# Performance work log

Measured on AMD Instinct MI355X. Metric: run time of the kernel, lower is better.

## Reference

```python
import jax, jax.numpy as jnp
import numpy as np

B, S, T, F, H, DEPTH = 8, 96, 96, 64, 64, 2


def setup_inputs() -> dict:
    key = jax.random.key(0)
    ks = jax.random.split(key, 10)
    scale = np.float32(1.0 / np.sqrt(H))
    rn = lambda k, sh: jax.random.normal(k, sh, dtype=jnp.float32)
    return {
        "src": rn(ks[0], (B, S, F)),
        "trg": rn(ks[1], (B, T, F)),
        "Wi_x": rn(ks[2], (DEPTH, F, H)) * scale,
        "Wh_x": rn(ks[3], (DEPTH, 2 * H, H)) * scale,
        "b_x": jnp.zeros((DEPTH, H), jnp.float32),
        "Wi_y": rn(ks[4], (DEPTH, F, H)) * scale,
        "Wh_y": rn(ks[5], (DEPTH, 2 * H, H)) * scale,
        "b_y": jnp.zeros((DEPTH, H), jnp.float32),
        "src_lens": jax.random.randint(ks[6], (B,), 1, S + 1),
        "trg_lens": jax.random.randint(ks[7], (B,), 1, T + 1),
    }


def _grid_layer(px, py, Whx, bx, Why, by):
    # px, py: (B, S, T, H) precomputed input projections (x @ Wi).
    # Wavefront recurrence: h_prev = [h_x(i-1,j), h_y(i,j-1)] (zeros at borders),
    # h_x(i,j) = tanh(px + h_prev @ Whx + bx), h_y(i,j) = tanh(py + h_prev @ Why + by).
    Bn, Sn, Tn, Hn = px.shape

    def row_step(hx_above_row, row_in):
        pxr, pyr = row_in  # (T, B, H) each

        def col_step(hy_left, col_in):
            pxc, pyc, hx_above = col_in  # (B, H) each
            h_prev = jnp.concatenate([hx_above, hy_left], axis=-1)  # (B, 2H)
            hx = jnp.tanh(pxc + h_prev @ Whx + bx)
            hy = jnp.tanh(pyc + h_prev @ Why + by)
            return hy, (hx, hy)

        _, (hx_row, hy_row) = jax.lax.scan(
            col_step, jnp.zeros((Bn, Hn), px.dtype), (pxr, pyr, hx_above_row))
        return hx_row, (hx_row, hy_row)

    px_t = jnp.transpose(px, (1, 2, 0, 3))  # (S, T, B, H)
    py_t = jnp.transpose(py, (1, 2, 0, 3))
    _, (hx, hy) = jax.lax.scan(
        row_step, jnp.zeros((Tn, Bn, Hn), px.dtype), (px_t, py_t))
    return jnp.transpose(hx, (2, 0, 1, 3)), jnp.transpose(hy, (2, 0, 1, 3))


def _forward(src, trg, Wi_x, Wh_x, b_x, Wi_y, Wh_y, b_y, src_lens, trg_lens):
    hx = hy = None
    hxs, hys = [], []
    for d in range(DEPTH):
        if d == 0:
            # depth 0: x input depends only on i, y input only on j
            px = jnp.broadcast_to((src @ Wi_x[0])[:, :, None, :], (B, S, T, H))
            py = jnp.broadcast_to((trg @ Wi_y[0])[:, None, :, :], (B, S, T, H))
        else:
            # depth d>0: inputs are previous depth's x/y outputs at the same (i,j)
            px = jnp.einsum('bsth,hk->bstk', hx, Wi_x[d])
            py = jnp.einsum('bsth,hk->bstk', hy, Wi_y[d])
        hx, hy = _grid_layer(px, py, Wh_x[d], b_x[d], Wh_y[d], b_y[d])
        hxs.append(hx)
        hys.append(hy)
    # zero out points outside each sample's (src_len x trg_len) valid grid
    mask = ((jnp.arange(S)[None, :, None] < src_lens[:, None, None])
            & (jnp.arange(T)[None, None, :] < trg_lens[:, None, None]))
    mask = mask[:, :, :, None].astype(src.dtype)  # (B, S, T, 1)
    out = jnp.stack([jnp.stack(hxs), jnp.stack(hys)])  # (2, DEPTH, B, S, T, H)
    return out * mask


_forward_jit = jax.jit(_forward)


def reference(src, trg, Wi_x, Wh_x, b_x, Wi_y, Wh_y, b_y, src_lens, trg_lens):
    return _forward_jit(src, trg, Wi_x, Wh_x, b_x, Wi_y, Wh_y, b_y,
                        src_lens, trg_lens)
```

## Files before the change

### kernel.cpp

```cpp
#include <hip/hip_runtime.h>

typedef unsigned short u16;
typedef unsigned int   u32;
typedef _Float16 f16x8 __attribute__((ext_vector_type(8)));
typedef float  f32x4  __attribute__((ext_vector_type(4)));
typedef int    i32x4  __attribute__((ext_vector_type(4)));
typedef u32    u32x2  __attribute__((ext_vector_type(2)));

#define Bn 8
#define Sn 96
#define Tn 96
#define Hn 64
#define H2n 128
#define STRB 144
#define ARRB 16384
#define LDSB (8*ARRB)

__device__ __forceinline__ int imax(int a, int b){ return a > b ? a : b; }
__device__ __forceinline__ int imin(int a, int b){ return a < b ? a : b; }

__device__ __forceinline__ u32 pack2f16(float a, float b){
  _Float16 ha = (_Float16)a, hb = (_Float16)b;
  return (u32)__builtin_bit_cast(u16, ha) | ((u32)__builtin_bit_cast(u16, hb) << 16);
}
__device__ __forceinline__ float fast_tanh(float x){
  float y = fminf(fmaxf(x * 2.88539008f, -30.f), 30.f);
  float e = __builtin_amdgcn_exp2f(y);
  return __builtin_fmaf(-2.f, __builtin_amdgcn_rcpf(e + 1.f), 1.f);
}
__device__ __forceinline__ void barrier_lds_only(){
  asm volatile("s_waitcnt vmcnt(63) expcnt(7) lgkmcnt(0)\n\ts_barrier" ::: "memory");
}

__global__ __launch_bounds__(64) void proj0_kernel(
  const float* __restrict__ src, const float* __restrict__ trg,
  const float* __restrict__ Wix, const float* __restrict__ Wiy,
  const float* __restrict__ bx, const float* __restrict__ by,
  float* __restrict__ ws)
{
  const int row = blockIdx.x, g = blockIdx.y, b = blockIdx.z;
  const int n = threadIdx.x;
  const float* x = (g == 0) ? (src + (b*Sn + row)*Hn) : (trg + (b*Tn + row)*Hn);
  const float* W = (g == 0) ? Wix : Wiy;
  float a = (g == 0) ? bx[n] : by[n];
  #pragma unroll 8
  for (int f = 0; f < Hn; ++f) a = fmaf(x[f], W[f*Hn + n], a);
  ws[((size_t)(b*2 + g)*Sn + row)*Hn + n] = a;
}

__global__ __launch_bounds__(1024, 1) void grid_rnn_fused(
  const float* __restrict__ Whx, const float* __restrict__ Why,
  const float* __restrict__ Wix, const float* __restrict__ Wiy,
  const float* __restrict__ bx,  const float* __restrict__ by,
  const int* __restrict__ src_lens, const int* __restrict__ trg_lens,
  float* __restrict__ out, const float* __restrict__ ws)
{
  extern __shared__ u16 smem[];
  char* const smemc = (char*)smem;
  const int b    = blockIdx.x;
  const int tid  = threadIdx.x;
  const int lane = tid & 63;
  const int wid  = __builtin_amdgcn_readfirstlane(tid >> 6);
  const int q    = lane >> 4;
  const int c    = lane & 15;
  const int dep  = wid & 1;
  const int nt   = (wid >> 1) & 3;
  const int g    = wid >> 3;
  const int sl = __builtin_amdgcn_readfirstlane(src_lens[b]);
  const int tl = __builtin_amdgcn_readfirstlane(trg_lens[b]);
  const int NB = sl + tl;

  for (int idx = tid; idx < LDSB/4; idx += 1024) ((u32*)smem)[idx] = 0u;

  const float* Wh = (g == 0 ? Whx : Why) + dep*H2n*Hn;
  const int nb = nt*16 + c;
  i32x4 whf[4];
  #pragma unroll
  for (int kk = 0; kk < 4; ++kk){
    #pragma unroll
    for (int p = 0; p < 4; ++p){
      float w0 = Wh[(kk*32 + q*8 + 2*p    )*Hn + nb];
      float w1 = Wh[(kk*32 + q*8 + 2*p + 1)*Hn + nb];
      whf[kk][p] = (int)pack2f16(w0, w1);
    }
  }
  const float* Wi = (g == 0 ? Wix : Wiy) + Hn*Hn;
  i32x4 wif[2];
  #pragma unroll
  for (int kk = 0; kk < 2; ++kk){
    #pragma unroll
    for (int p = 0; p < 4; ++p){
      float w0 = Wi[(kk*32 + q*8 + 2*p    )*Hn + nb];
      float w1 = Wi[(kk*32 + q*8 + 2*p + 1)*Hn + nb];
      wif[kk][p] = (int)pack2f16(w0, w1);
    }
  }
  f32x4 bias4;
  {
    const float* bb = (g == 0 ? bx : by) + dep*Hn;
    #pragma unroll
    for (int r4 = 0; r4 < 4; ++r4) bias4[r4] = bb[nt*16 + q*4 + r4];
  }
  const char* const pxb = (const char*)(ws + (size_t)(b*2 + g)*Sn*Hn);
  char* const outb = (char*)(out + (size_t)((g*2 + dep)*Bn + b)*(size_t)(Sn*Tn)*Hn);

  const int plJ = q*16 - c*STRB;
  const int plI = q*16 + c*STRB;
  const int plP = g ? plI : plJ;
  const int plW = (g ? c*STRB : -c*STRB) + nt*32 + q*8;
  const int plO = c*24320 + nt*64 + q*16;
  const int plPx= (g ? -c*256 : c*256) + nt*64 + q*16;

  const int baseX = dep*4*ARRB;
  const int baseY = dep*4*ARRB + 2*ARRB;
  const int baseP = g ? 2*ARRB : 0;
  const int baseW = dep*4*ARRB + (g ? 2*ARRB : 0);

  __syncthreads();

  for (int r = 0; r < NB; ++r){
    const int myd  = r - dep;
    const bool wact = (myd >= 0) && (myd <= NB - 2);
    const int cpB = (r & 1) ? ARRB : 0;
    const int ppB = ARRB - cpB;
    const int i0 = imax(0, myd - (tl - 1));
    const int i1 = imin(sl - 1, myd);
    const int nc = i1 - i0 + 1;
    const int mtiles = (nc + 15) >> 4;
    const int sJ = (myd - i0)*STRB;
    const int sI = i0*STRB;
    const int aX  = baseX + ppB + sJ;
    const int loX = baseX + ppB + (myd - i1)*STRB;
    const int aY  = baseY + ppB + sI;
    const int hiY = baseY + ppB + i1*STRB + 48;
    const int aP  = baseP + ppB + (g ? sI : sJ);
    const int loP = baseP + ppB + (g ? sI : (myd - i1)*STRB);
    const int hiP = baseP + ppB + (g ? i1*STRB : sJ) + 48;
    const int aW  = baseW + cpB + (g ? sI : sJ);
    const int sO  = myd*256 + i0*24320;
    const int sPx = (g ? (myd - i0) : i0)*256;
    const int pxLo= (g ? (myd - i1) : i0)*256;
    const int pxHi= (g ? (myd - i0) : i1)*256 + 240;

    #pragma unroll
    for (int u = 0; u < 6; ++u){
      if (!(wact && u < mtiles)) continue;
      const int du = u*2304;
      int vX = aX - du + plJ; vX = imax(vX, loX);
      int vY = aY + du + plI; vY = imin(vY, hiY);

      f32x4 acc;
      if (dep == 0){
        int vp = (g ? sPx - u*4096 : sPx + u*4096) + plPx;
        vp = imin(imax(vp, pxLo), pxHi);
        acc = *(const f32x4*)(pxb + (u32)vp);
      } else {
        acc = bias4;
      }
      #pragma unroll
      for (int kk = 0; kk < 2; ++kk){
        i32x4 sv = *(const i32x4*)(smemc + (vX + kk*64));
        acc = __builtin_amdgcn_mfma_f32_16x16x32_f16(
                __builtin_bit_cast(f16x8, whf[kk]),
                __builtin_bit_cast(f16x8, sv), acc, 0, 0, 0);
      }
      #pragma unroll
      for (int kk = 0; kk < 2; ++kk){
        i32x4 sv = *(const i32x4*)(smemc + (vY + kk*64));
        acc = __builtin_amdgcn_mfma_f32_16x16x32_f16(
                __builtin_bit_cast(f16x8, whf[kk+2]),
                __builtin_bit_cast(f16x8, sv), acc, 0, 0, 0);
      }
      if (dep == 1){
        int vP = aP + (g ? du : -du) + plP;
        vP = imin(imax(vP, loP), hiP);
        #pragma unroll
        for (int kk = 0; kk < 2; ++kk){
          i32x4 pv = *(const i32x4*)(smemc + (vP + kk*64));
          acc = __builtin_amdgcn_mfma_f32_16x16x32_f16(
                  __builtin_bit_cast(f16x8, wif[kk]),
                  __builtin_bit_cast(f16x8, pv), acc, 0, 0, 0);
        }
      }
      float h0 = fast_tanh(acc[0]), h1 = fast_tanh(acc[1]);
      float h2 = fast_tanh(acc[2]), h3 = fast_tanh(acc[3]);
      if (c < nc - u*16){
        int vW = aW + (g ? du : -du) + plW;
        u32x2 hp; hp[0] = pack2f16(h0, h1); hp[1] = pack2f16(h2, h3);
        *(u32x2*)(smemc + vW) = hp;
        int vO = sO + u*389120 + plO;
        f32x4 ov = {h0, h1, h2, h3};
        *(f32x4*)(outb + (u32)vO) = ov;
      }
    }
    barrier_lds_only();
  }
}

extern "C" void kernel_launch(void* const* d_in, const int* in_sizes, int n_in,
                              void* d_out, int out_size, void* d_ws, size_t ws_size,
                              hipStream_t stream) {
  (void)in_sizes; (void)n_in; (void)ws_size;
  (void)hipFuncSetAttribute((const void*)grid_rnn_fused,
                            hipFuncAttributeMaxDynamicSharedMemorySize, LDSB);
  (void)hipMemsetAsync(d_out, 0, (size_t)out_size, stream);
  proj0_kernel<<<dim3(Sn, 2, Bn), 64, 0, stream>>>(
      (const float*)d_in[0], (const float*)d_in[1],
      (const float*)d_in[2], (const float*)d_in[5],
      (const float*)d_in[4], (const float*)d_in[7],
      (float*)d_ws);
  grid_rnn_fused<<<dim3(Bn), dim3(1024), LDSB, stream>>>(
      (const float*)d_in[3], (const float*)d_in[6],
      (const float*)d_in[2], (const float*)d_in[5],
      (const float*)d_in[4], (const float*)d_in[7],
      (const int*)d_in[8], (const int*)d_in[9],
      (float*)d_out, (const float*)d_ws);
}
```

Before: 526.8 us.

## Switch wavefront recurrence to 32x32x16 MFMA tiles with 512-thread blocks

Replaces the 16x16x32 MFMA tiling, where each wave computed a 16-column slice of one cell batch, with 32x32x16 MFMA tiles in which each wave computes all 64 outputs for 32 diagonal cells. The block shrinks from 16 to 8 waves, each wave alternating between tiles. The LDS row stride moves to 152 bytes and state is read with paired 8-byte loads, aiming to cut bank conflicts. The clamp in tanh is dropped. The goal is fewer MFMA instructions and fewer redundant state loads per step, at the cost of more registers per wave, less wave-level parallelism and lower MFMA utilisation on short diagonals.

```diff
diff --git a/kernel.cpp b/kernel.cpp
--- a/kernel.cpp
+++ b/kernel.cpp
@@ -4,6 +4,7 @@
 typedef unsigned int   u32;
 typedef _Float16 f16x8 __attribute__((ext_vector_type(8)));
 typedef float  f32x4  __attribute__((ext_vector_type(4)));
+typedef float  f32x16 __attribute__((ext_vector_type(16)));
 typedef int    i32x4  __attribute__((ext_vector_type(4)));
 typedef u32    u32x2  __attribute__((ext_vector_type(2)));
 
@@ -12,9 +13,10 @@
 #define Tn 96
 #define Hn 64
 #define H2n 128
-#define STRB 144
+#define STRB 152
 #define ARRB 16384
 #define LDSB (8*ARRB)
+#define ODS 24320
 
 __device__ __forceinline__ int imax(int a, int b){ return a > b ? a : b; }
 __device__ __forceinline__ int imin(int a, int b){ return a < b ? a : b; }
@@ -24,12 +26,17 @@
   return (u32)__builtin_bit_cast(u16, ha) | ((u32)__builtin_bit_cast(u16, hb) << 16);
 }
 __device__ __forceinline__ float fast_tanh(float x){
-  float y = fminf(fmaxf(x * 2.88539008f, -30.f), 30.f);
-  float e = __builtin_amdgcn_exp2f(y);
+  float e = exp2f(x * 2.88539008f);
   return __builtin_fmaf(-2.f, __builtin_amdgcn_rcpf(e + 1.f), 1.f);
 }
 __device__ __forceinline__ void barrier_lds_only(){
   asm volatile("s_waitcnt vmcnt(63) expcnt(7) lgkmcnt(0)\n\ts_barrier" ::: "memory");
+}
+__device__ __forceinline__ f16x8 ld_state(const char* p){
+  u32x2 a = *(const u32x2*)(p);
+  u32x2 b = *(const u32x2*)(p + 8);
+  i32x4 v; v[0] = (int)a[0]; v[1] = (int)a[1]; v[2] = (int)b[0]; v[3] = (int)b[1];
+  return __builtin_bit_cast(f16x8, v);
 }
 
 __global__ __launch_bounds__(64) void proj0_kernel(
@@ -48,7 +55,7 @@
   ws[((size_t)(b*2 + g)*Sn + row)*Hn + n] = a;
 }
 
-__global__ __launch_bounds__(1024, 1) void grid_rnn_fused(
+__global__ __launch_bounds__(512, 2) void grid_rnn_fused(
   const float* __restrict__ Whx, const float* __restrict__ Why,
   const float* __restrict__ Wix, const float* __restrict__ Wiy,
   const float* __restrict__ bx,  const float* __restrict__ by,
@@ -61,60 +68,63 @@
   const int tid  = threadIdx.x;
   const int lane = tid & 63;
   const int wid  = __builtin_amdgcn_readfirstlane(tid >> 6);
-  const int q    = lane >> 4;
-  const int c    = lane & 15;
+  const int c32  = lane & 31;
+  const int hi   = lane >> 5;
   const int dep  = wid & 1;
-  const int nt   = (wid >> 1) & 3;
-  const int g    = wid >> 3;
+  const int g    = (wid >> 1) & 1;
+  const int ct   = (wid >> 2) & 1;
   const int sl = __builtin_amdgcn_readfirstlane(src_lens[b]);
   const int tl = __builtin_amdgcn_readfirstlane(trg_lens[b]);
   const int NB = sl + tl;
 
-  for (int idx = tid; idx < LDSB/4; idx += 1024) ((u32*)smem)[idx] = 0u;
+  for (int idx = tid; idx < LDSB/4; idx += 512) ((u32*)smem)[idx] = 0u;
 
   const float* Wh = (g == 0 ? Whx : Why) + dep*H2n*Hn;
-  const int nb = nt*16 + c;
-  i32x4 whf[4];
+  i32x4 whf[8][2];
   #pragma unroll
-  for (int kk = 0; kk < 4; ++kk){
-    #pragma unroll
-    for (int p = 0; p < 4; ++p){
-      float w0 = Wh[(kk*32 + q*8 + 2*p    )*Hn + nb];
-      float w1 = Wh[(kk*32 + q*8 + 2*p + 1)*Hn + nb];
-      whf[kk][p] = (int)pack2f16(w0, w1);
-    }
-  }
-  const float* Wi = (g == 0 ? Wix : Wiy) + Hn*Hn;
-  i32x4 wif[2];
-  #pragma unroll
-  for (int kk = 0; kk < 2; ++kk){
-    #pragma unroll
-    for (int p = 0; p < 4; ++p){
-      float w0 = Wi[(kk*32 + q*8 + 2*p    )*Hn + nb];
-      float w1 = Wi[(kk*32 + q*8 + 2*p + 1)*Hn + nb];
-      wif[kk][p] = (int)pack2f16(w0, w1);
-    }
-  }
-  f32x4 bias4;
-  {
-    const float* bb = (g == 0 ? bx : by) + dep*Hn;
-    #pragma unroll
-    for (int r4 = 0; r4 < 4; ++r4) bias4[r4] = bb[nt*16 + q*4 + r4];
+  for (int kk = 0; kk < 8; ++kk)
+    #pragma unroll
+    for (int mt = 0; mt < 2; ++mt)
+      #pragma unroll
+      for (int p = 0; p < 4; ++p){
+        float w0 = Wh[(kk*16 + hi*8 + 2*p    )*Hn + mt*32 + c32];
+        float w1 = Wh[(kk*16 + hi*8 + 2*p + 1)*Hn + mt*32 + c32];
+        whf[kk][mt][p] = (int)pack2f16(w0, w1);
+      }
+  i32x4 wif[4][2];
+  f32x16 biasr[2];
+  if (dep == 1){
+    const float* Wi = (g == 0 ? Wix : Wiy) + Hn*Hn;
+    #pragma unroll
+    for (int kk = 0; kk < 4; ++kk)
+      #pragma unroll
+      for (int mt = 0; mt < 2; ++mt)
+        #pragma unroll
+        for (int p = 0; p < 4; ++p){
+          float w0 = Wi[(kk*16 + hi*8 + 2*p    )*Hn + mt*32 + c32];
+          float w1 = Wi[(kk*16 + hi*8 + 2*p + 1)*Hn + mt*32 + c32];
+          wif[kk][mt][p] = (int)pack2f16(w0, w1);
+        }
+    const float* bb = (g == 0 ? bx : by) + Hn;
+    #pragma unroll
+    for (int mt = 0; mt < 2; ++mt)
+      #pragma unroll
+      for (int reg = 0; reg < 16; ++reg)
+        biasr[mt][reg] = bb[mt*32 + (reg & 3) + 8*(reg >> 2) + 4*hi];
   }
   const char* const pxb = (const char*)(ws + (size_t)(b*2 + g)*Sn*Hn);
   char* const outb = (char*)(out + (size_t)((g*2 + dep)*Bn + b)*(size_t)(Sn*Tn)*Hn);
 
-  const int plJ = q*16 - c*STRB;
-  const int plI = q*16 + c*STRB;
-  const int plP = g ? plI : plJ;
-  const int plW = (g ? c*STRB : -c*STRB) + nt*32 + q*8;
-  const int plO = c*24320 + nt*64 + q*16;
-  const int plPx= (g ? -c*256 : c*256) + nt*64 + q*16;
-
-  const int baseX = dep*4*ARRB;
-  const int baseY = dep*4*ARRB + 2*ARRB;
-  const int baseP = g ? 2*ARRB : 0;
-  const int baseW = dep*4*ARRB + (g ? 2*ARRB : 0);
+  const int plX  = -c32*STRB + hi*16;
+  const int plY  =  c32*STRB + hi*16;
+  const int plP  = g ? plY : plX;
+  const int plW  = (g ? c32*STRB : -c32*STRB) + hi*8;
+  const int plO  = c32*ODS + hi*16;
+  const int plPx = (g ? -c32*256 : c32*256) + hi*16;
+
+  const int depB  = dep*4*ARRB;
+  const int basePg = g ? 2*ARRB : 0;
+  const int baseWg = depB + (g ? 2*ARRB : 0);
 
   __syncthreads();
 
@@ -126,71 +136,88 @@
     const int i0 = imax(0, myd - (tl - 1));
     const int i1 = imin(sl - 1, myd);
     const int nc = i1 - i0 + 1;
-    const int mtiles = (nc + 15) >> 4;
-    const int sJ = (myd - i0)*STRB;
-    const int sI = i0*STRB;
-    const int aX  = baseX + ppB + sJ;
-    const int loX = baseX + ppB + (myd - i1)*STRB;
-    const int aY  = baseY + ppB + sI;
-    const int hiY = baseY + ppB + i1*STRB + 48;
-    const int aP  = baseP + ppB + (g ? sI : sJ);
-    const int loP = baseP + ppB + (g ? sI : (myd - i1)*STRB);
-    const int hiP = baseP + ppB + (g ? i1*STRB : sJ) + 48;
-    const int aW  = baseW + cpB + (g ? sI : sJ);
-    const int sO  = myd*256 + i0*24320;
-    const int sPx = (g ? (myd - i0) : i0)*256;
-    const int pxLo= (g ? (myd - i1) : i0)*256;
-    const int pxHi= (g ? (myd - i0) : i1)*256 + 240;
-
-    #pragma unroll
-    for (int u = 0; u < 6; ++u){
-      if (!(wact && u < mtiles)) continue;
-      const int du = u*2304;
-      int vX = aX - du + plJ; vX = imax(vX, loX);
-      int vY = aY + du + plI; vY = imin(vY, hiY);
-
-      f32x4 acc;
+    const int mt32 = (nc + 31) >> 5;
+    const int rJ0 = myd - i0, rJm = myd - i1;
+    const int aX  = depB + ppB + rJ0*STRB;
+    const int loX = depB + ppB + rJm*STRB;
+    const int aY  = depB + 2*ARRB + ppB + i0*STRB;
+    const int hiY = depB + 2*ARRB + ppB + i1*STRB + 16;
+    const int aP  = basePg + ppB + (g ? i0 : rJ0)*STRB;
+    const int loP = basePg + ppB + (g ? i0 : rJm)*STRB;
+    const int hiP = basePg + ppB + (g ? i1 : rJ0)*STRB + 16;
+    const int aW  = baseWg + cpB + (g ? i0 : rJ0)*STRB;
+    const int sO  = myd*256 + i0*ODS;
+    const int sPx = (g ? rJ0 : i0)*256;
+    const int loPx= (g ? rJm : i0)*256;
+    const int hiPx= (g ? rJ0 : i1)*256 + 16;
+
+    #pragma unroll
+    for (int t = 0; t < 2; ++t){
+      const int u = ct + 2*t;
+      if (!(wact && u < mt32)) continue;
+      const int cb = u*32;
+
+      int vX = aX - cb*STRB + plX; vX = imax(vX, loX);
+      int vY = aY + cb*STRB + plY; vY = imin(vY, hiY);
+
+      f32x16 acc[2];
       if (dep == 0){
-        int vp = (g ? sPx - u*4096 : sPx + u*4096) + plPx;
-        vp = imin(imax(vp, pxLo), pxHi);
-        acc = *(const f32x4*)(pxb + (u32)vp);
+        int vp = sPx + (g ? -(cb*256) : cb*256) + plPx;
+        vp = imin(imax(vp, loPx), hiPx);
+        #pragma unroll
+        for (int m = 0; m < 4; ++m){
+          f32x4 t0 = *(const f32x4*)(pxb + (u32)vp + m*32);
+          f32x4 t1 = *(const f32x4*)(pxb + (u32)vp + 128 + m*32);
+          #pragma unroll
+          for (int e = 0; e < 4; ++e){ acc[0][4*m+e] = t0[e]; acc[1][4*m+e] = t1[e]; }
+        }
       } else {
-        acc = bias4;
-      }
-      #pragma unroll
-      for (int kk = 0; kk < 2; ++kk){
-        i32x4 sv = *(const i32x4*)(smemc + (vX + kk*64));
-        acc = __builtin_amdgcn_mfma_f32_16x16x32_f16(
-                __builtin_bit_cast(f16x8, whf[kk]),
-                __builtin_bit_cast(f16x8, sv), acc, 0, 0, 0);
-      }
-      #pragma unroll
-      for (int kk = 0; kk < 2; ++kk){
-        i32x4 sv = *(const i32x4*)(smemc + (vY + kk*64));
-        acc = __builtin_amdgcn_mfma_f32_16x16x32_f16(
-                __builtin_bit_cast(f16x8, whf[kk+2]),
-                __builtin_bit_cast(f16x8, sv), acc, 0, 0, 0);
+        acc[0] = biasr[0]; acc[1] = biasr[1];
+      }
+      #pragma unroll
+      for (int kk = 0; kk < 4; ++kk){
+        f16x8 bv = ld_state(smemc + vX + kk*32);
+        acc[0] = __builtin_amdgcn_mfma_f32_32x32x16_f16(
+                   __builtin_bit_cast(f16x8, whf[kk][0]), bv, acc[0], 0, 0, 0);
+        acc[1] = __builtin_amdgcn_mfma_f32_32x32x16_f16(
+                   __builtin_bit_cast(f16x8, whf[kk][1]), bv, acc[1], 0, 0, 0);
+      }
+      #pragma unroll
+      for (int kk = 0; kk < 4; ++kk){
+        f16x8 bv = ld_state(smemc + vY + kk*32);
+        acc[0] = __builtin_amdgcn_mfma_f32_32x32x16_f16(
+                   __builtin_bit_cast(f16x8, whf[kk+4][0]), bv, acc[0], 0, 0, 0);
+        acc[1] = __builtin_amdgcn_mfma_f32_32x32x16_f16(
+                   __builtin_bit_cast(f16x8, whf[kk+4][1]), bv, acc[1], 0, 0, 0);
       }
       if (dep == 1){
-        int vP = aP + (g ? du : -du) + plP;
+        int vP = aP + (g ? cb*STRB : -(cb*STRB)) + plP;
         vP = imin(imax(vP, loP), hiP);
         #pragma unroll
-        for (int kk = 0; kk < 2; ++kk){
-          i32x4 pv = *(const i32x4*)(smemc + (vP + kk*64));
-          acc = __builtin_amdgcn_mfma_f32_16x16x32_f16(
-                  __builtin_bit_cast(f16x8, wif[kk]),
-                  __builtin_bit_cast(f16x8, pv), acc, 0, 0, 0);
+        for (int kk = 0; kk < 4; ++kk){
+          f16x8 pv = ld_state(smemc + vP + kk*32);
+          acc[0] = __builtin_amdgcn_mfma_f32_32x32x16_f16(
+                     __builtin_bit_cast(f16x8, wif[kk][0]), pv, acc[0], 0, 0, 0);
+          acc[1] = __builtin_amdgcn_mfma_f32_32x32x16_f16(
+                     __builtin_bit_cast(f16x8, wif[kk][1]), pv, acc[1], 0, 0, 0);
         }
       }
-      float h0 = fast_tanh(acc[0]), h1 = fast_tanh(acc[1]);
-      float h2 = fast_tanh(acc[2]), h3 = fast_tanh(acc[3]);
-      if (c < nc - u*16){
-        int vW = aW + (g ? du : -du) + plW;
-        u32x2 hp; hp[0] = pack2f16(h0, h1); hp[1] = pack2f16(h2, h3);
-        *(u32x2*)(smemc + vW) = hp;
-        int vO = sO + u*389120 + plO;
-        f32x4 ov = {h0, h1, h2, h3};
-        *(f32x4*)(outb + (u32)vO) = ov;
+      if (c32 < nc - cb){
+        const int vW = aW + (g ? cb*STRB : -(cb*STRB)) + plW;
+        const int vO = sO + cb*ODS + plO;
+        #pragma unroll
+        for (int mt = 0; mt < 2; ++mt)
+          #pragma unroll
+          for (int m = 0; m < 4; ++m){
+            float h0 = fast_tanh(acc[mt][4*m+0]);
+            float h1 = fast_tanh(acc[mt][4*m+1]);
+            float h2 = fast_tanh(acc[mt][4*m+2]);
+            float h3 = fast_tanh(acc[mt][4*m+3]);
+            u32x2 hp; hp[0] = pack2f16(h0, h1); hp[1] = pack2f16(h2, h3);
+            *(u32x2*)(smemc + vW + mt*64 + m*16) = hp;
+            f32x4 ov = {h0, h1, h2, h3};
+            *(f32x4*)(outb + (u32)vO + mt*128 + m*32) = ov;
+          }
       }
     }
     barrier_lds_only();
@@ -209,7 +236,7 @@
       (const float*)d_in[2], (const float*)d_in[5],
       (const float*)d_in[4], (const float*)d_in[7],
       (float*)d_ws);
-  grid_rnn_fused<<<dim3(Bn), dim3(1024), LDSB, stream>>>(
+  grid_rnn_fused<<<dim3(Bn), dim3(512), LDSB, stream>>>(
       (const float*)d_in[3], (const float*)d_in[6],
       (const float*)d_in[2], (const float*)d_in[5],
       (const float*)d_in[4], (const float*)d_in[7],
```

After: 608.8 us. +15.6%, slower.

## Stage depth-0 input projections in LDS as fp16 and pad state stride

Applied to the files above, without the earlier changes.

The depth-0 input projections are copied once from the workspace into LDS as packed fp16 rows, and the wavefront loop reads them from LDS instead of global memory. The LDS state row stride changes from 144 to 152 bytes, which alters bank mapping. tanh drops its input clamp and uses exp2f. Rounding px to fp16 adds precision loss, and removing the clamp depends on exp2f overflowing to infinity and rcp of infinity giving zero.

```diff
diff --git a/kernel.cpp b/kernel.cpp
--- a/kernel.cpp
+++ b/kernel.cpp
@@ -3,6 +3,7 @@
 typedef unsigned short u16;
 typedef unsigned int   u32;
 typedef _Float16 f16x8 __attribute__((ext_vector_type(8)));
+typedef float  f32x2  __attribute__((ext_vector_type(2)));
 typedef float  f32x4  __attribute__((ext_vector_type(4)));
 typedef int    i32x4  __attribute__((ext_vector_type(4)));
 typedef u32    u32x2  __attribute__((ext_vector_type(2)));
@@ -12,9 +13,15 @@
 #define Tn 96
 #define Hn 64
 #define H2n 128
-#define STRB 144
+#define STRB 152
 #define ARRB 16384
-#define LDSB (8*ARRB)
+#define STATEB 131072
+#define PXROW 152
+#define PXG   (Sn*PXROW)
+#define PXBASE STATEB
+#define LDSB  (STATEB + 2*PXG)
+#define ODS 24320
+#define TSTP 2432
 
 __device__ __forceinline__ int imax(int a, int b){ return a > b ? a : b; }
 __device__ __forceinline__ int imin(int a, int b){ return a < b ? a : b; }
@@ -23,9 +30,11 @@
   _Float16 ha = (_Float16)a, hb = (_Float16)b;
   return (u32)__builtin_bit_cast(u16, ha) | ((u32)__builtin_bit_cast(u16, hb) << 16);
 }
+__device__ __forceinline__ float f16tof(u32 v){
+  return (float)__builtin_bit_cast(_Float16, (u16)v);
+}
 __device__ __forceinline__ float fast_tanh(float x){
-  float y = fminf(fmaxf(x * 2.88539008f, -30.f), 30.f);
-  float e = __builtin_amdgcn_exp2f(y);
+  float e = exp2f(x * 2.88539008f);
   return __builtin_fmaf(-2.f, __builtin_amdgcn_rcpf(e + 1.f), 1.f);
 }
 __device__ __forceinline__ void barrier_lds_only(){
@@ -70,51 +79,60 @@
   const int tl = __builtin_amdgcn_readfirstlane(trg_lens[b]);
   const int NB = sl + tl;
 
-  for (int idx = tid; idx < LDSB/4; idx += 1024) ((u32*)smem)[idx] = 0u;
+  for (int idx = tid; idx < STATEB/16; idx += 1024) ((i32x4*)smem)[idx] = (i32x4)(0);
+
+  {
+    const int gp = tid >> 9;
+    const int t5 = tid & 511;
+    const float* wsg = ws + (size_t)(b*2 + gp)*Sn*Hn;
+    #pragma unroll
+    for (int it = 0; it < 6; ++it){
+      int w = t5 + it*512;
+      int row = w >> 5, pr = w & 31;
+      f32x2 v = *(const f32x2*)(wsg + row*64 + pr*2);
+      *(u32*)(smemc + PXBASE + gp*PXG + row*PXROW + pr*4) = pack2f16(v[0], v[1]);
+    }
+  }
 
   const float* Wh = (g == 0 ? Whx : Why) + dep*H2n*Hn;
   const int nb = nt*16 + c;
   i32x4 whf[4];
   #pragma unroll
-  for (int kk = 0; kk < 4; ++kk){
+  for (int kk = 0; kk < 4; ++kk)
     #pragma unroll
     for (int p = 0; p < 4; ++p){
       float w0 = Wh[(kk*32 + q*8 + 2*p    )*Hn + nb];
       float w1 = Wh[(kk*32 + q*8 + 2*p + 1)*Hn + nb];
       whf[kk][p] = (int)pack2f16(w0, w1);
     }
-  }
   const float* Wi = (g == 0 ? Wix : Wiy) + Hn*Hn;
   i32x4 wif[2];
   #pragma unroll
-  for (int kk = 0; kk < 2; ++kk){
+  for (int kk = 0; kk < 2; ++kk)
     #pragma unroll
     for (int p = 0; p < 4; ++p){
       float w0 = Wi[(kk*32 + q*8 + 2*p    )*Hn + nb];
       float w1 = Wi[(kk*32 + q*8 + 2*p + 1)*Hn + nb];
       wif[kk][p] = (int)pack2f16(w0, w1);
     }
-  }
   f32x4 bias4;
   {
     const float* bb = (g == 0 ? bx : by) + dep*Hn;
     #pragma unroll
     for (int r4 = 0; r4 < 4; ++r4) bias4[r4] = bb[nt*16 + q*4 + r4];
   }
-  const char* const pxb = (const char*)(ws + (size_t)(b*2 + g)*Sn*Hn);
   char* const outb = (char*)(out + (size_t)((g*2 + dep)*Bn + b)*(size_t)(Sn*Tn)*Hn);
 
-  const int plJ = q*16 - c*STRB;
-  const int plI = q*16 + c*STRB;
-  const int plP = g ? plI : plJ;
-  const int plW = (g ? c*STRB : -c*STRB) + nt*32 + q*8;
-  const int plO = c*24320 + nt*64 + q*16;
-  const int plPx= (g ? -c*256 : c*256) + nt*64 + q*16;
-
-  const int baseX = dep*4*ARRB;
-  const int baseY = dep*4*ARRB + 2*ARRB;
-  const int baseP = g ? 2*ARRB : 0;
-  const int baseW = dep*4*ARRB + (g ? 2*ARRB : 0);
+  const int plX  = q*16 - c*STRB;
+  const int plY  = q*16 + c*STRB;
+  const int plP  = g ? plY : plX;
+  const int plW  = (g ? c*STRB : -c*STRB) + nt*32 + q*8;
+  const int plPx = (g ? -c*PXROW : c*PXROW) + nt*32 + q*8;
+  const int plO  = c*ODS + nt*64 + q*16;
+
+  const int depB   = dep*4*ARRB;
+  const int basePg = g ? 2*ARRB : 0;
+  const int baseWg = depB + (g ? 2*ARRB : 0);
 
   __syncthreads();
 
@@ -127,33 +145,35 @@
     const int i1 = imin(sl - 1, myd);
     const int nc = i1 - i0 + 1;
     const int mtiles = (nc + 15) >> 4;
-    const int sJ = (myd - i0)*STRB;
-    const int sI = i0*STRB;
-    const int aX  = baseX + ppB + sJ;
-    const int loX = baseX + ppB + (myd - i1)*STRB;
-    const int aY  = baseY + ppB + sI;
-    const int hiY = baseY + ppB + i1*STRB + 48;
-    const int aP  = baseP + ppB + (g ? sI : sJ);
-    const int loP = baseP + ppB + (g ? sI : (myd - i1)*STRB);
-    const int hiP = baseP + ppB + (g ? i1*STRB : sJ) + 48;
-    const int aW  = baseW + cpB + (g ? sI : sJ);
-    const int sO  = myd*256 + i0*24320;
-    const int sPx = (g ? (myd - i0) : i0)*256;
-    const int pxLo= (g ? (myd - i1) : i0)*256;
-    const int pxHi= (g ? (myd - i0) : i1)*256 + 240;
+    const int rJ0 = myd - i0, rJm = myd - i1;
+    const int aX  = depB + ppB + rJ0*STRB;
+    const int loX = depB + ppB + rJm*STRB;
+    const int aY  = depB + 2*ARRB + ppB + i0*STRB;
+    const int hiY = depB + 2*ARRB + ppB + i1*STRB + 48;
+    const int aP  = basePg + ppB + (g ? i0 : rJ0)*STRB;
+    const int loP = basePg + ppB + (g ? i0 : rJm)*STRB;
+    const int hiP = basePg + ppB + (g ? i1 : rJ0)*STRB + 48;
+    const int aW  = baseWg + cpB + (g ? i0 : rJ0)*STRB;
+    const int aPx = PXBASE + g*PXG + (g ? rJ0 : i0)*PXROW;
+    const int loPx= PXBASE + g*PXG + (g ? rJm : i0)*PXROW;
+    const int hiPx= PXBASE + g*PXG + (g ? rJ0 : i1)*PXROW + 120;
+    const int sO  = myd*256 + i0*ODS;
 
     #pragma unroll
     for (int u = 0; u < 6; ++u){
       if (!(wact && u < mtiles)) continue;
-      const int du = u*2304;
-      int vX = aX - du + plJ; vX = imax(vX, loX);
-      int vY = aY + du + plI; vY = imin(vY, hiY);
+      const int du = u*TSTP;
+
+      int vX = aX - du + plX; vX = imax(vX, loX);
+      int vY = aY + du + plY; vY = imin(vY, hiY);
 
       f32x4 acc;
       if (dep == 0){
-        int vp = (g ? sPx - u*4096 : sPx + u*4096) + plPx;
-        vp = imin(imax(vp, pxLo), pxHi);
-        acc = *(const f32x4*)(pxb + (u32)vp);
+        int vp = aPx + (g ? -du : du) + plPx;
+        vp = imin(imax(vp, loPx), hiPx);
+        u32x2 pv = *(const u32x2*)(smemc + vp);
+        acc[0] = f16tof(pv[0] & 0xffffu); acc[1] = f16tof(pv[0] >> 16);
+        acc[2] = f16tof(pv[1] & 0xffffu); acc[3] = f16tof(pv[1] >> 16);
       } else {
         acc = bias4;
       }
@@ -185,12 +205,11 @@
       float h0 = fast_tanh(acc[0]), h1 = fast_tanh(acc[1]);
       float h2 = fast_tanh(acc[2]), h3 = fast_tanh(acc[3]);
       if (c < nc - u*16){
-        int vW = aW + (g ? du : -du) + plW;
+        const int vW = aW + (g ? du : -du) + plW;
         u32x2 hp; hp[0] = pack2f16(h0, h1); hp[1] = pack2f16(h2, h3);
         *(u32x2*)(smemc + vW) = hp;
-        int vO = sO + u*389120 + plO;
         f32x4 ov = {h0, h1, h2, h3};
-        *(f32x4*)(outb + (u32)vO) = ov;
+        *(f32x4*)(outb + (u32)(sO + u*(16*ODS) + plO)) = ov;
       }
     }
     barrier_lds_only();
```

Measured after the change: 1.381 ms. 2.62x slower.
